# Optimization experiments

Measured on AMD Instinct MI355X. Metric: run time of the kernel, lower is better.

Reference implementation:

```python
import jax, jax.numpy as jnp
import numpy as np

T, B, I, H, FC, C = 256, 256, 1024, 256, 128, 8  # seq, batch, input, hidden, fc1, classes


def setup_inputs() -> dict:
    key = jax.random.key(0)
    ks = jax.random.split(key, 9)
    s_ih = 1.0 / np.sqrt(H)
    return {
        "x": jax.random.normal(ks[0], (T, B, I), dtype=jnp.float32),
        "W_ih": jax.random.uniform(ks[1], (4 * H, I), jnp.float32, -s_ih, s_ih),
        "W_hh": jax.random.uniform(ks[2], (4 * H, H), jnp.float32, -s_ih, s_ih),
        "b_ih": jax.random.uniform(ks[3], (4 * H,), jnp.float32, -s_ih, s_ih),
        "b_hh": jax.random.uniform(ks[4], (4 * H,), jnp.float32, -s_ih, s_ih),
        "W1": jax.random.uniform(ks[5], (FC, H), jnp.float32, -s_ih, s_ih),
        "b1": jax.random.uniform(ks[6], (FC,), jnp.float32, -s_ih, s_ih),
        "W2": jax.random.uniform(ks[7], (C, FC), jnp.float32, -1.0 / np.sqrt(FC), 1.0 / np.sqrt(FC)),
        "b2": jax.random.uniform(ks[8], (C,), jnp.float32, -1.0 / np.sqrt(FC), 1.0 / np.sqrt(FC)),
    }


def _lstm(x, W_ih, W_hh, b_ih, b_hh):
    # x: [T, B, I]; PyTorch gate order: i, f, g, o
    xg = jnp.einsum("tbi,gi->tbg", x, W_ih) + b_ih + b_hh  # precompute input projections [T,B,4H]

    def step(carry, xg_t):
        h, c = carry
        z = xg_t + h @ W_hh.T  # [B, 4H]
        i, f, g, o = jnp.split(z, 4, axis=-1)
        i = jax.nn.sigmoid(i)
        f = jax.nn.sigmoid(f)
        g = jnp.tanh(g)
        o = jax.nn.sigmoid(o)
        c = f * c + i * g
        h = o * jnp.tanh(c)
        return (h, c), h

    h0 = jnp.zeros((x.shape[1], W_hh.shape[1]), x.dtype)
    (hn, cn), out = jax.lax.scan(step, (h0, h0), xg)
    return out  # [T, B, H]


def reference(x, W_ih, W_hh, b_ih, b_hh, W1, b1, W2, b2):
    out = _lstm(x, W_ih, W_hh, b_ih, b_hh)      # [T, B, H]
    out = jax.nn.relu(out)
    out = jax.nn.relu(out @ W1.T + b1)           # [T, B, 128]
    out = out @ W2.T + b2                        # [T, B, num_classes]
    return out
```

## Files before the change

kernel.cpp:

```cpp
#include <hip/hip_runtime.h>
#include <type_traits>


typedef float    f4    __attribute__((ext_vector_type(4)));
typedef float    f32x4 __attribute__((ext_vector_type(4)));
typedef _Float16 h8    __attribute__((ext_vector_type(8)));
typedef _Float16 h4    __attribute__((ext_vector_type(4)));

__device__ __forceinline__ float ldf(const float* p)    { return *p; }
__device__ __forceinline__ float ldf(const _Float16* p) { return (float)*p; }

__device__ __forceinline__ float fast_sigmoid(float x) {
    return 1.f / (1.f + __expf(-x));
}
__device__ __forceinline__ float fast_tanh(float x) {
    const float e = __expf(-2.f * fabsf(x));
    const float t = (1.f - e) / (1.f + e);
    return copysignf(t, x);
}

__device__ __forceinline__ f32x4 ld_pin(const _Float16* p) {
    f32x4 d;
    asm volatile("global_load_dwordx4 %0, %1, off\n\t"
                 "s_waitcnt vmcnt(0)"
                 : "=v"(d) : "v"(p) : "memory");
    return d;
}

__global__ __launch_bounds__(256) void k_bias(const float* __restrict__ b_ih,
                                              const float* __restrict__ b_hh,
                                              float* __restrict__ bias) {
    const int i = blockIdx.x * 256 + threadIdx.x;
    if (i < 1024) bias[i] = b_ih[i] + b_hh[i];
}

__global__ __launch_bounds__(256) void k_pack(const float* __restrict__ W_hh,
                                              _Float16* __restrict__ Wp) {
    const int idx = blockIdx.x * 256 + threadIdx.x;
    const int fi = idx >> 6;
    const int l  = idx & 63;
    const int g  = (fi >> 3) * 16 + (l & 15);
    const int k  = (fi & 7) * 32 + ((l >> 4) << 3);
    const float* src = &W_hh[(size_t)g * 256 + k];
    h8 v;
    #pragma unroll
    for (int c = 0; c < 8; ++c) v[c] = (_Float16)src[c];
    *(h8*)&Wp[(size_t)idx * 8] = v;
}

__global__ __launch_bounds__(256) void k_xg_mfma(
    const float* __restrict__ x, const float* __restrict__ W_ih,
    const float* __restrict__ bias, _Float16* __restrict__ xg2)
{
    __shared__ _Float16 As[2][128][40];
    __shared__ _Float16 Bs[2][128][40];
    const int tid = threadIdx.x;
    const int l   = tid & 63;
    const int w   = tid >> 6;
    const int m0  = blockIdx.y * 128;
    const int n0  = blockIdx.x * 128;
    const int wr  = (w >> 1) * 64;
    const int wc  = (w & 1) * 64;
    const int srow = tid >> 2;
    const int skof = (tid & 3) * 8;
    const int lr = l & 15;
    const int lg = l >> 4;

    f32x4 acc[4][4] = {};
    f4 ldA[2][2], ldB[2][2];

    auto XG_LOAD = [&](int kt) {
        const int k0 = kt * 32;
        #pragma unroll
        for (int s = 0; s < 2; ++s) {
            const float* xa = &x[(size_t)(m0 + srow + s * 64) * 1024 + k0 + skof];
            const float* wb = &W_ih[(size_t)(n0 + srow + s * 64) * 1024 + k0 + skof];
            ldA[s][0] = *(const f4*)xa; ldA[s][1] = *(const f4*)(xa + 4);
            ldB[s][0] = *(const f4*)wb; ldB[s][1] = *(const f4*)(wb + 4);
        }
    };
    auto XG_WRITE = [&](int buf) {
        #pragma unroll
        for (int s = 0; s < 2; ++s) {
            h8 va, vb;
            #pragma unroll
            for (int c = 0; c < 8; ++c) {
                va[c] = (_Float16)ldA[s][c >> 2][c & 3];
                vb[c] = (_Float16)ldB[s][c >> 2][c & 3];
            }
            *(h8*)&As[buf][srow + s * 64][skof] = va;
            *(h8*)&Bs[buf][srow + s * 64][skof] = vb;
        }
    };

    XG_LOAD(0);
    XG_WRITE(0);
    __syncthreads();
    for (int kt = 0; kt < 32; ++kt) {
        const int cur = kt & 1;
        if (kt + 1 < 32) XG_LOAD(kt + 1);
        h8 af[4], bf[4];
        #pragma unroll
        for (int mf = 0; mf < 4; ++mf) af[mf] = *(const h8*)&As[cur][wr + mf * 16 + lr][lg * 8];
        #pragma unroll
        for (int nf = 0; nf < 4; ++nf) bf[nf] = *(const h8*)&Bs[cur][wc + nf * 16 + lr][lg * 8];
        #pragma unroll
        for (int mf = 0; mf < 4; ++mf)
            #pragma unroll
            for (int nf = 0; nf < 4; ++nf)
                acc[mf][nf] = __builtin_amdgcn_mfma_f32_16x16x32_f16(af[mf], bf[nf], acc[mf][nf], 0, 0, 0);
        if (kt + 1 < 32) XG_WRITE((kt + 1) & 1);
        __syncthreads();
    }
    #pragma unroll
    for (int nf = 0; nf < 4; ++nf) {
        const int col  = n0 + wc + nf * 16 + lr;
        const float bv = bias[col];
        const int gate = col >> 8;
        const int w8   = (col >> 5) & 7;
        const int jt   = (col >> 4) & 1;
        #pragma unroll
        for (int mf = 0; mf < 4; ++mf) {
            const int rowb = m0 + wr + mf * 16 + lg * 4;
            const int tt = rowb >> 8;
            const int gb = (rowb >> 4) & 15;
            h4 pk;
            #pragma unroll
            for (int r = 0; r < 4; ++r) pk[r] = (_Float16)(acc[mf][nf][r] + bv);
            *(h4*)&xg2[((((size_t)tt * 16 + gb) * 8 + w8) * 64 + l) * 32 + gate * 8 + jt * 4] = pk;
        }
    }
}

__global__ __launch_bounds__(512, 2) void k_lstm_8w(
    const _Float16* __restrict__ xg2, const _Float16* __restrict__ Wp,
    _Float16* __restrict__ h_all)
{
    __shared__ _Float16 wlds[8 * 17 * 512];
    __shared__ _Float16 h_sh[2][16][264];
    const int tid = threadIdx.x;
    const int w  = tid >> 6;
    const int l  = tid & 63;
    const int lr = l & 15;
    const int lg = l >> 4;
    const int g  = blockIdx.x;
    const int b0 = g * 16;

    auto fgid = [&](int ti, int kb) {
        return (((ti >> 1) * 16 + w * 2 + (ti & 1)) * 8 + kb);
    };
    auto ldfrag = [&](int ti, int kb) {
        return *(const h8*)&Wp[((size_t)fgid(ti, kb) * 64 + l) * 8];
    };

    f32x4 wpin[16];
    #pragma unroll
    for (int kb = 0; kb < 2; ++kb)
        #pragma unroll
        for (int ti = 0; ti < 8; ++ti)
            wpin[kb * 8 + ti] = ld_pin(&Wp[((size_t)fgid(ti, kb) * 64 + l) * 8]);

    #pragma unroll
    for (int ti = 0; ti < 8; ++ti)
        *(h8*)&wlds[((w * 17 + ti) * 64 + l) * 8] = ldfrag(ti, 2);
    #pragma unroll
    for (int ti = 0; ti < 8; ++ti)
        *(h8*)&wlds[((w * 17 + 8 + ti) * 64 + l) * 8] = ldfrag(ti, 3);
    *(h8*)&wlds[((w * 17 + 16) * 64 + l) * 8] = ldfrag(0, 4);

    {
        _Float16* p = &h_sh[0][0][0];
        for (int i = tid; i < 2 * 16 * 264; i += 512) p[i] = (_Float16)0.f;
    }
    __syncthreads();

    float c[8];
    #pragma unroll
    for (int i = 0; i < 8; ++i) c[i] = 0.f;

    h8 xq[4];
    {
        const size_t E0 = (((size_t)g * 8 + w) * 64 + l) * 32;
        #pragma unroll
        for (int q = 0; q < 4; ++q) xq[q] = *(const h8*)&xg2[E0 + q * 8];
    }

    for (int t = 0; t < 256; ++t) {
        const int cur = t & 1;
        const int nxt = cur ^ 1;

        f32x4 acc[8];
        #pragma unroll
        for (int ti = 0; ti < 8; ++ti) {
            #pragma unroll
            for (int r = 0; r < 4; ++r)
                acc[ti][r] = (float)xq[ti >> 1][(ti & 1) * 4 + r];
        }

        h8 xqn[4];
        if (t < 255) {
            const size_t En = ((((size_t)(t + 1) * 16 + g) * 8 + w) * 64 + l) * 32;
            #pragma unroll
            for (int q = 0; q < 4; ++q) xqn[q] = *(const h8*)&xg2[En + q * 8];
        }

        unsigned sA = 0;
        asm volatile("" : "+v"(sA));
        h8 sv4[7], sv5[8];
        #pragma unroll
        for (int ti = 1; ti < 8; ++ti)
            sv4[ti - 1] = *(const h8*)&Wp[((size_t)fgid(ti, 4) * 64 + l) * 8 + sA];
        #pragma unroll
        for (int ti = 0; ti < 8; ++ti)
            sv5[ti] = *(const h8*)&Wp[((size_t)fgid(ti, 5) * 64 + l) * 8 + sA];

        {
            h8 av = *(const h8*)&h_sh[cur][lr][0 * 32 + lg * 8];
            #pragma unroll
            for (int ti = 0; ti < 8; ++ti)
                acc[ti] = __builtin_amdgcn_mfma_f32_16x16x32_f16(av, __builtin_bit_cast(h8, wpin[ti]), acc[ti], 0, 0, 0);
            av = *(const h8*)&h_sh[cur][lr][1 * 32 + lg * 8];
            #pragma unroll
            for (int ti = 0; ti < 8; ++ti)
                acc[ti] = __builtin_amdgcn_mfma_f32_16x16x32_f16(av, __builtin_bit_cast(h8, wpin[8 + ti]), acc[ti], 0, 0, 0);
        }

        unsigned sB = 0;
        asm volatile("" : "+v"(sB));
        h8 sv6[8];
        #pragma unroll
        for (int ti = 0; ti < 8; ++ti)
            sv6[ti] = *(const h8*)&Wp[((size_t)fgid(ti, 6) * 64 + l) * 8 + sB];

        {
            h8 av = *(const h8*)&h_sh[cur][lr][2 * 32 + lg * 8];
            #pragma unroll
            for (int ti = 0; ti < 8; ++ti) {
                const h8 b = *(const h8*)&wlds[((w * 17 + ti) * 64 + l) * 8];
                acc[ti] = __builtin_amdgcn_mfma_f32_16x16x32_f16(av, b, acc[ti], 0, 0, 0);
            }
            av = *(const h8*)&h_sh[cur][lr][3 * 32 + lg * 8];
            #pragma unroll
            for (int ti = 0; ti < 8; ++ti) {
                const h8 b = *(const h8*)&wlds[((w * 17 + 8 + ti) * 64 + l) * 8];
                acc[ti] = __builtin_amdgcn_mfma_f32_16x16x32_f16(av, b, acc[ti], 0, 0, 0);
            }
        }

        {
            h8 av = *(const h8*)&h_sh[cur][lr][4 * 32 + lg * 8];
            {
                const h8 b = *(const h8*)&wlds[((w * 17 + 16) * 64 + l) * 8];
                acc[0] = __builtin_amdgcn_mfma_f32_16x16x32_f16(av, b, acc[0], 0, 0, 0);
            }
            #pragma unroll
            for (int ti = 1; ti < 8; ++ti)
                acc[ti] = __builtin_amdgcn_mfma_f32_16x16x32_f16(av, sv4[ti - 1], acc[ti], 0, 0, 0);
            av = *(const h8*)&h_sh[cur][lr][5 * 32 + lg * 8];
            #pragma unroll
            for (int ti = 0; ti < 8; ++ti)
                acc[ti] = __builtin_amdgcn_mfma_f32_16x16x32_f16(av, sv5[ti], acc[ti], 0, 0, 0);
        }

        unsigned sC = 0;
        asm volatile("" : "+v"(sC));
        h8 sv7[8];
        #pragma unroll
        for (int ti = 0; ti < 8; ++ti)
            sv7[ti] = *(const h8*)&Wp[((size_t)fgid(ti, 7) * 64 + l) * 8 + sC];

        {
            h8 av = *(const h8*)&h_sh[cur][lr][6 * 32 + lg * 8];
            #pragma unroll
            for (int ti = 0; ti < 8; ++ti)
                acc[ti] = __builtin_amdgcn_mfma_f32_16x16x32_f16(av, sv6[ti], acc[ti], 0, 0, 0);
            av = *(const h8*)&h_sh[cur][lr][7 * 32 + lg * 8];
            #pragma unroll
            for (int ti = 0; ti < 8; ++ti)
                acc[ti] = __builtin_amdgcn_mfma_f32_16x16x32_f16(av, sv7[ti], acc[ti], 0, 0, 0);
        }

        #pragma unroll
        for (int jt = 0; jt < 2; ++jt) {
            #pragma unroll
            for (int r = 0; r < 4; ++r) {
                const float ig = fast_sigmoid(acc[0 * 2 + jt][r]);
                const float fg = fast_sigmoid(acc[1 * 2 + jt][r]);
                const float gg = fast_tanh(acc[2 * 2 + jt][r]);
                const float og = fast_sigmoid(acc[3 * 2 + jt][r]);
                const int ci = jt * 4 + r;
                c[ci] = fg * c[ci] + ig * gg;
                const float hv = og * fast_tanh(c[ci]);
                const _Float16 h16 = (_Float16)hv;
                h_sh[nxt][lg * 4 + r][w * 32 + jt * 16 + lr] = h16;
                h_all[((size_t)t * 256 + b0 + lg * 4 + r) * 256 + w * 32 + jt * 16 + lr] = h16;
            }
        }

        if (t < 255) {
            #pragma unroll
            for (int q = 0; q < 4; ++q) xq[q] = xqn[q];
        }

        asm volatile("s_waitcnt lgkmcnt(0)" ::: "memory");
        __builtin_amdgcn_s_barrier();
        __builtin_amdgcn_sched_barrier(0);
    }
}

template <typename HT>
__global__ __launch_bounds__(256) void k_fc(
    const HT* __restrict__ h_all, const float* __restrict__ W1,
    const float* __restrict__ b1, const float* __restrict__ W2,
    const float* __restrict__ b2, float* __restrict__ out)
{
    __shared__ __align__(16) float smem[12288];
    float* hsT = smem;
    float* w1T = smem + 4096;
    const int tid = threadIdx.x;
    const int m0 = blockIdx.x * 64;
    const int tx = tid & 15;
    const int ty = tid >> 4;
    const int r0 = ty * 4;
    const int fA = tx * 4;
    const int fB = 64 + tx * 4;
    float acc[4][8] = {};
    for (int kc = 0; kc < 4; ++kc) {
        const int k0 = kc * 64;
        __syncthreads();
        #pragma unroll
        for (int i = 0; i < 4; ++i) {
            const int fid = tid + i * 256;
            const int rr = fid >> 4;
            const int qq = fid & 15;
            const HT* p = &h_all[(size_t)(m0 + rr) * 256 + k0 + qq * 4];
            f4 v;
            if constexpr (std::is_same<HT, float>::value) {
                v = *(const f4*)p;
            } else {
                v[0] = ldf(p); v[1] = ldf(p + 1); v[2] = ldf(p + 2); v[3] = ldf(p + 3);
            }
            #pragma unroll
            for (int cc = 0; cc < 4; ++cc)
                hsT[(qq * 4 + cc) * 64 + rr] = fmaxf(v[cc], 0.f);
        }
        #pragma unroll
        for (int i = 0; i < 8; ++i) {
            const int fid = tid + i * 256;
            const int ff = fid >> 4;
            const int qq = fid & 15;
            const f4 v = *(const f4*)&W1[(size_t)ff * 256 + k0 + qq * 4];
            #pragma unroll
            for (int cc = 0; cc < 4; ++cc)
                w1T[(qq * 4 + cc) * 128 + ff] = v[cc];
        }
        __syncthreads();
        #pragma unroll 4
        for (int kk = 0; kk < 64; ++kk) {
            const f4 aa = *(const f4*)&hsT[kk * 64 + r0];
            const f4 ba = *(const f4*)&w1T[kk * 128 + fA];
            const f4 bb = *(const f4*)&w1T[kk * 128 + fB];
            #pragma unroll
            for (int i = 0; i < 4; ++i) {
                #pragma unroll
                for (int j = 0; j < 4; ++j) {
                    acc[i][j]     = fmaf(aa[i], ba[j], acc[i][j]);
                    acc[i][j + 4] = fmaf(aa[i], bb[j], acc[i][j + 4]);
                }
            }
        }
    }
    __syncthreads();
    float* fc1s = smem;
    #pragma unroll
    for (int j = 0; j < 4; ++j) {
        const float bbA = b1[fA + j];
        const float bbB = b1[fB + j];
        #pragma unroll
        for (int i = 0; i < 4; ++i) {
            fc1s[(r0 + i) * 132 + fA + j] = fmaxf(acc[i][j] + bbA, 0.f);
            fc1s[(r0 + i) * 132 + fB + j] = fmaxf(acc[i][j + 4] + bbB, 0.f);
        }
    }
    __syncthreads();
    const int r  = tid >> 2;
    const int c0 = (tid & 3) * 2;
    float o0 = b2[c0], o1 = b2[c0 + 1];
    #pragma unroll
    for (int fq = 0; fq < 32; ++fq) {
        const f4 p  = *(const f4*)&fc1s[r * 132 + fq * 4];
        const f4 wa = *(const f4*)&W2[(size_t)c0 * 128 + fq * 4];
        const f4 wb = *(const f4*)&W2[(size_t)(c0 + 1) * 128 + fq * 4];
        o0 += p[0] * wa[0] + p[1] * wa[1] + p[2] * wa[2] + p[3] * wa[3];
        o1 += p[0] * wb[0] + p[1] * wb[1] + p[2] * wb[2] + p[3] * wb[3];
    }
    out[(size_t)(m0 + r) * 8 + c0]     = o0;
    out[(size_t)(m0 + r) * 8 + c0 + 1] = o1;
}

extern "C" void kernel_launch(void* const* d_in, const int* in_sizes, int n_in,
                              void* d_out, int out_size, void* d_ws, size_t ws_size,
                              hipStream_t stream)
{
    const float* x    = (const float*)d_in[0];
    const float* W_ih = (const float*)d_in[1];
    const float* W_hh = (const float*)d_in[2];
    const float* b_ih = (const float*)d_in[3];
    const float* b_hh = (const float*)d_in[4];
    const float* W1   = (const float*)d_in[5];
    const float* b1   = (const float*)d_in[6];
    const float* W2   = (const float*)d_in[7];
    const float* b2   = (const float*)d_in[8];
    float* out = (float*)d_out;
    char* ws = (char*)d_ws;

    _Float16* xg2   = (_Float16*)ws;
    _Float16* h_all = (_Float16*)(ws + 134217728);
    _Float16* Wp    = (_Float16*)(ws + 167772160);
    float*    bias  = (float*)   (ws + 168296448);

    k_bias<<<4, 256, 0, stream>>>(b_ih, b_hh, bias);
    k_pack<<<128, 256, 0, stream>>>(W_hh, Wp);
    k_xg_mfma<<<dim3(8, 512), 256, 0, stream>>>(x, W_ih, bias, xg2);
    k_lstm_8w<<<16, 512, 0, stream>>>(xg2, Wp, h_all);
    k_fc<_Float16><<<1024, 256, 0, stream>>>(h_all, W1, b1, W2, b2, out);
}
```

Before: 2.029 ms.

## Split LSTM recurrence across 16 waves per block instead of 8

The recurrent kernel now runs 1024 threads (16 waves) per batch group. Each wave owns 16 hidden units, so it keeps 4 gate accumulators instead of 8. The xg2 layout written by the input-projection GEMM is reorganised to match the new per-wave fragment ownership. The W_hh fragment split between LDS, pinned registers and per-step global loads is rebalanced (kb0-1 in LDS, kb2 pinned, kb3-7 streamed). This halves the serial MFMA chain per wave each timestep, at the cost of a larger block barrier and more waves contending for the same CU.

After: 2.113 ms. +4.1%, slower.

```diff
diff --git a/kernel.cpp b/kernel.cpp
--- a/kernel.cpp
+++ b/kernel.cpp
@@ -117,8 +117,7 @@
         const int col  = n0 + wc + nf * 16 + lr;
         const float bv = bias[col];
         const int gate = col >> 8;
-        const int w8   = (col >> 5) & 7;
-        const int jt   = (col >> 4) & 1;
+        const int w16  = (col >> 4) & 15;
         #pragma unroll
         for (int mf = 0; mf < 4; ++mf) {
             const int rowb = m0 + wr + mf * 16 + lg * 4;
@@ -127,16 +126,16 @@
             h4 pk;
             #pragma unroll
             for (int r = 0; r < 4; ++r) pk[r] = (_Float16)(acc[mf][nf][r] + bv);
-            *(h4*)&xg2[((((size_t)tt * 16 + gb) * 8 + w8) * 64 + l) * 32 + gate * 8 + jt * 4] = pk;
-        }
-    }
-}
-
-__global__ __launch_bounds__(512, 2) void k_lstm_8w(
+            *(h4*)&xg2[((((size_t)tt * 16 + gb) * 16 + w16) * 64 + l) * 16 + gate * 4] = pk;
+        }
+    }
+}
+
+__global__ __launch_bounds__(1024, 4) void k_lstm_16w(
     const _Float16* __restrict__ xg2, const _Float16* __restrict__ Wp,
     _Float16* __restrict__ h_all)
 {
-    __shared__ _Float16 wlds[8 * 17 * 512];
+    __shared__ _Float16 wlds[16 * 8 * 512];
     __shared__ _Float16 h_sh[2][16][264];
     const int tid = threadIdx.x;
     const int w  = tid >> 6;
@@ -146,161 +145,141 @@
     const int g  = blockIdx.x;
     const int b0 = g * 16;
 
-    auto fgid = [&](int ti, int kb) {
-        return (((ti >> 1) * 16 + w * 2 + (ti & 1)) * 8 + kb);
+    auto fgid = [&](int gate, int kb) { return ((gate * 16 + w) * 8 + kb); };
+    auto ldfrag = [&](int gate, int kb) {
+        return *(const h8*)&Wp[((size_t)fgid(gate, kb) * 64 + l) * 8];
     };
-    auto ldfrag = [&](int ti, int kb) {
-        return *(const h8*)&Wp[((size_t)fgid(ti, kb) * 64 + l) * 8];
-    };
-
-    f32x4 wpin[16];
-    #pragma unroll
-    for (int kb = 0; kb < 2; ++kb)
-        #pragma unroll
-        for (int ti = 0; ti < 8; ++ti)
-            wpin[kb * 8 + ti] = ld_pin(&Wp[((size_t)fgid(ti, kb) * 64 + l) * 8]);
-
-    #pragma unroll
-    for (int ti = 0; ti < 8; ++ti)
-        *(h8*)&wlds[((w * 17 + ti) * 64 + l) * 8] = ldfrag(ti, 2);
-    #pragma unroll
-    for (int ti = 0; ti < 8; ++ti)
-        *(h8*)&wlds[((w * 17 + 8 + ti) * 64 + l) * 8] = ldfrag(ti, 3);
-    *(h8*)&wlds[((w * 17 + 16) * 64 + l) * 8] = ldfrag(0, 4);
+
+    #pragma unroll
+    for (int gate = 0; gate < 4; ++gate)
+        #pragma unroll
+        for (int kb = 0; kb < 2; ++kb)
+            *(h8*)&wlds[((w * 8 + gate * 2 + kb) * 64 + l) * 8] = ldfrag(gate, kb);
+
+    f32x4 wpin[4];
+    #pragma unroll
+    for (int gate = 0; gate < 4; ++gate)
+        wpin[gate] = ld_pin(&Wp[((size_t)fgid(gate, 2) * 64 + l) * 8]);
 
     {
         _Float16* p = &h_sh[0][0][0];
-        for (int i = tid; i < 2 * 16 * 264; i += 512) p[i] = (_Float16)0.f;
+        for (int i = tid; i < 2 * 16 * 264; i += 1024) p[i] = (_Float16)0.f;
     }
     __syncthreads();
 
-    float c[8];
-    #pragma unroll
-    for (int i = 0; i < 8; ++i) c[i] = 0.f;
-
-    h8 xq[4];
+    float c[4] = {0.f, 0.f, 0.f, 0.f};
+
+    h8 xq0, xq1;
     {
-        const size_t E0 = (((size_t)g * 8 + w) * 64 + l) * 32;
-        #pragma unroll
-        for (int q = 0; q < 4; ++q) xq[q] = *(const h8*)&xg2[E0 + q * 8];
+        const size_t E0 = (((size_t)g * 16 + w) * 64 + l) * 16;
+        xq0 = *(const h8*)&xg2[E0];
+        xq1 = *(const h8*)&xg2[E0 + 8];
     }
 
     for (int t = 0; t < 256; ++t) {
         const int cur = t & 1;
         const int nxt = cur ^ 1;
 
-        f32x4 acc[8];
-        #pragma unroll
-        for (int ti = 0; ti < 8; ++ti) {
-            #pragma unroll
-            for (int r = 0; r < 4; ++r)
-                acc[ti][r] = (float)xq[ti >> 1][(ti & 1) * 4 + r];
-        }
-
-        h8 xqn[4];
+        f32x4 acc[4];
+        #pragma unroll
+        for (int gate = 0; gate < 4; ++gate) {
+            #pragma unroll
+            for (int r = 0; r < 4; ++r) {
+                const int v = gate * 4 + r;
+                acc[gate][r] = (float)((v < 8) ? xq0[v & 7] : xq1[v & 7]);
+            }
+        }
+
+        h8 xqn0, xqn1;
         if (t < 255) {
-            const size_t En = ((((size_t)(t + 1) * 16 + g) * 8 + w) * 64 + l) * 32;
-            #pragma unroll
-            for (int q = 0; q < 4; ++q) xqn[q] = *(const h8*)&xg2[En + q * 8];
+            const size_t En = ((((size_t)(t + 1) * 16 + g) * 16 + w) * 64 + l) * 16;
+            xqn0 = *(const h8*)&xg2[En];
+            xqn1 = *(const h8*)&xg2[En + 8];
         }
 
         unsigned sA = 0;
         asm volatile("" : "+v"(sA));
-        h8 sv4[7], sv5[8];
-        #pragma unroll
-        for (int ti = 1; ti < 8; ++ti)
-            sv4[ti - 1] = *(const h8*)&Wp[((size_t)fgid(ti, 4) * 64 + l) * 8 + sA];
-        #pragma unroll
-        for (int ti = 0; ti < 8; ++ti)
-            sv5[ti] = *(const h8*)&Wp[((size_t)fgid(ti, 5) * 64 + l) * 8 + sA];
-
+        h8 sv3[4], sv4[4];
+        #pragma unroll
+        for (int gate = 0; gate < 4; ++gate)
+            sv3[gate] = *(const h8*)&Wp[((size_t)fgid(gate, 3) * 64 + l) * 8 + sA];
+        #pragma unroll
+        for (int gate = 0; gate < 4; ++gate)
+            sv4[gate] = *(const h8*)&Wp[((size_t)fgid(gate, 4) * 64 + l) * 8 + sA];
+
+        #pragma unroll
+        for (int kb = 0; kb < 2; ++kb) {
+            const h8 av = *(const h8*)&h_sh[cur][lr][kb * 32 + lg * 8];
+            #pragma unroll
+            for (int gate = 0; gate < 4; ++gate) {
+                const h8 b = *(const h8*)&wlds[((w * 8 + gate * 2 + kb) * 64 + l) * 8];
+                acc[gate] = __builtin_amdgcn_mfma_f32_16x16x32_f16(av, b, acc[gate], 0, 0, 0);
+            }
+        }
         {
-            h8 av = *(const h8*)&h_sh[cur][lr][0 * 32 + lg * 8];
-            #pragma unroll
-            for (int ti = 0; ti < 8; ++ti)
-                acc[ti] = __builtin_amdgcn_mfma_f32_16x16x32_f16(av, __builtin_bit_cast(h8, wpin[ti]), acc[ti], 0, 0, 0);
-            av = *(const h8*)&h_sh[cur][lr][1 * 32 + lg * 8];
-            #pragma unroll
-            for (int ti = 0; ti < 8; ++ti)
-                acc[ti] = __builtin_amdgcn_mfma_f32_16x16x32_f16(av, __builtin_bit_cast(h8, wpin[8 + ti]), acc[ti], 0, 0, 0);
+            const h8 av = *(const h8*)&h_sh[cur][lr][2 * 32 + lg * 8];
+            #pragma unroll
+            for (int gate = 0; gate < 4; ++gate)
+                acc[gate] = __builtin_amdgcn_mfma_f32_16x16x32_f16(av, __builtin_bit_cast(h8, wpin[gate]), acc[gate], 0, 0, 0);
         }
 
         unsigned sB = 0;
         asm volatile("" : "+v"(sB));
-        h8 sv6[8];
-        #pragma unroll
-        for (int ti = 0; ti < 8; ++ti)
-            sv6[ti] = *(const h8*)&Wp[((size_t)fgid(ti, 6) * 64 + l) * 8 + sB];
+        h8 sv5[4], sv6[4];
+        #pragma unroll
+        for (int gate = 0; gate < 4; ++gate)
+            sv5[gate] = *(const h8*)&Wp[((size_t)fgid(gate, 5) * 64 + l) * 8 + sB];
+        #pragma unroll
+        for (int gate = 0; gate < 4; ++gate)
+            sv6[gate] = *(const h8*)&Wp[((size_t)fgid(gate, 6) * 64 + l) * 8 + sB];
 
         {
-            h8 av = *(const h8*)&h_sh[cur][lr][2 * 32 + lg * 8];
-            #pragma unroll
-            for (int ti = 0; ti < 8; ++ti) {
-                const h8 b = *(const h8*)&wlds[((w * 17 + ti) * 64 + l) * 8];
-                acc[ti] = __builtin_amdgcn_mfma_f32_16x16x32_f16(av, b, acc[ti], 0, 0, 0);
-            }
-            av = *(const h8*)&h_sh[cur][lr][3 * 32 + lg * 8];
-            #pragma unroll
-            for (int ti = 0; ti < 8; ++ti) {
-                const h8 b = *(const h8*)&wlds[((w * 17 + 8 + ti) * 64 + l) * 8];
-                acc[ti] = __builtin_amdgcn_mfma_f32_16x16x32_f16(av, b, acc[ti], 0, 0, 0);
-            }
-        }
-
-        {
-            h8 av = *(const h8*)&h_sh[cur][lr][4 * 32 + lg * 8];
-            {
-                const h8 b = *(const h8*)&wlds[((w * 17 + 16) * 64 + l) * 8];
-                acc[0] = __builtin_amdgcn_mfma_f32_16x16x32_f16(av, b, acc[0], 0, 0, 0);
-            }
-            #pragma unroll
-            for (int ti = 1; ti < 8; ++ti)
-                acc[ti] = __builtin_amdgcn_mfma_f32_16x16x32_f16(av, sv4[ti - 1], acc[ti], 0, 0, 0);
-            av = *(const h8*)&h_sh[cur][lr][5 * 32 + lg * 8];
-            #pragma unroll
-            for (int ti = 0; ti < 8; ++ti)
-                acc[ti] = __builtin_amdgcn_mfma_f32_16x16x32_f16(av, sv5[ti], acc[ti], 0, 0, 0);
+            h8 av = *(const h8*)&h_sh[cur][lr][3 * 32 + lg * 8];
+            #pragma unroll
+            for (int gate = 0; gate < 4; ++gate)
+                acc[gate] = __builtin_amdgcn_mfma_f32_16x16x32_f16(av, sv3[gate], acc[gate], 0, 0, 0);
+            av = *(const h8*)&h_sh[cur][lr][4 * 32 + lg * 8];
+            #pragma unroll
+            for (int gate = 0; gate < 4; ++gate)
+                acc[gate] = __builtin_amdgcn_mfma_f32_16x16x32_f16(av, sv4[gate], acc[gate], 0, 0, 0);
         }
 
         unsigned sC = 0;
         asm volatile("" : "+v"(sC));
-        h8 sv7[8];
-        #pragma unroll
-        for (int ti = 0; ti < 8; ++ti)
-            sv7[ti] = *(const h8*)&Wp[((size_t)fgid(ti, 7) * 64 + l) * 8 + sC];
+        h8 sv7[4];
+        #pragma unroll
+        for (int gate = 0; gate < 4; ++gate)
+            sv7[gate] = *(const h8*)&Wp[((size_t)fgid(gate, 7) * 64 + l) * 8 + sC];
 
         {
-            h8 av = *(const h8*)&h_sh[cur][lr][6 * 32 + lg * 8];
-            #pragma unroll
-            for (int ti = 0; ti < 8; ++ti)
-                acc[ti] = __builtin_amdgcn_mfma_f32_16x16x32_f16(av, sv6[ti], acc[ti], 0, 0, 0);
+            h8 av = *(const h8*)&h_sh[cur][lr][5 * 32 + lg * 8];
+            #pragma unroll
+            for (int gate = 0; gate < 4; ++gate)
+                acc[gate] = __builtin_amdgcn_mfma_f32_16x16x32_f16(av, sv5[gate], acc[gate], 0, 0, 0);
+            av = *(const h8*)&h_sh[cur][lr][6 * 32 + lg * 8];
+            #pragma unroll
+            for (int gate = 0; gate < 4; ++gate)
+                acc[gate] = __builtin_amdgcn_mfma_f32_16x16x32_f16(av, sv6[gate], acc[gate], 0, 0, 0);
             av = *(const h8*)&h_sh[cur][lr][7 * 32 + lg * 8];
             #pragma unroll
-            for (int ti = 0; ti < 8; ++ti)
-                acc[ti] = __builtin_amdgcn_mfma_f32_16x16x32_f16(av, sv7[ti], acc[ti], 0, 0, 0);
-        }
-
-        #pragma unroll
-        for (int jt = 0; jt < 2; ++jt) {
-            #pragma unroll
-            for (int r = 0; r < 4; ++r) {
-                const float ig = fast_sigmoid(acc[0 * 2 + jt][r]);
-                const float fg = fast_sigmoid(acc[1 * 2 + jt][r]);
-                const float gg = fast_tanh(acc[2 * 2 + jt][r]);
-                const float og = fast_sigmoid(acc[3 * 2 + jt][r]);
-                const int ci = jt * 4 + r;
-                c[ci] = fg * c[ci] + ig * gg;
-                const float hv = og * fast_tanh(c[ci]);
-                const _Float16 h16 = (_Float16)hv;
-                h_sh[nxt][lg * 4 + r][w * 32 + jt * 16 + lr] = h16;
-                h_all[((size_t)t * 256 + b0 + lg * 4 + r) * 256 + w * 32 + jt * 16 + lr] = h16;
-            }
-        }
-
-        if (t < 255) {
-            #pragma unroll
-            for (int q = 0; q < 4; ++q) xq[q] = xqn[q];
-        }
+            for (int gate = 0; gate < 4; ++gate)
+                acc[gate] = __builtin_amdgcn_mfma_f32_16x16x32_f16(av, sv7[gate], acc[gate], 0, 0, 0);
+        }
+
+        #pragma unroll
+        for (int r = 0; r < 4; ++r) {
+            const float ig = fast_sigmoid(acc[0][r]);
+            const float fg = fast_sigmoid(acc[1][r]);
+            const float gg = fast_tanh(acc[2][r]);
+            const float og = fast_sigmoid(acc[3][r]);
+            c[r] = fg * c[r] + ig * gg;
+            const float hv = og * fast_tanh(c[r]);
+            const _Float16 h16 = (_Float16)hv;
+            h_sh[nxt][lg * 4 + r][w * 16 + lr] = h16;
+            h_all[((size_t)t * 256 + b0 + lg * 4 + r) * 256 + w * 16 + lr] = h16;
+        }
+
+        if (t < 255) { xq0 = xqn0; xq1 = xqn1; }
 
         asm volatile("s_waitcnt lgkmcnt(0)" ::: "memory");
         __builtin_amdgcn_s_barrier();
@@ -422,6 +401,6 @@
     k_bias<<<4, 256, 0, stream>>>(b_ih, b_hh, bias);
     k_pack<<<128, 256, 0, stream>>>(W_hh, Wp);
     k_xg_mfma<<<dim3(8, 512), 256, 0, stream>>>(x, W_ih, bias, xg2);
-    k_lstm_8w<<<16, 512, 0, stream>>>(xg2, Wp, h_all);
+    k_lstm_16w<<<16, 1024, 0, stream>>>(xg2, Wp, h_all);
     k_fc<_Float16><<<1024, 256, 0, stream>>>(h_all, W1, b1, W2, b2, out);
 }
```
